# Kernel optimization log

Measured on AMD Instinct MI355X. Metric: run time of the kernel, lower is better.

## Reference

```python
import jax, jax.numpy as jnp
import numpy as np

N_NODES = 50000
N_EDGES = 800000
IN_FEATS = 128
NUM_HEADS = 4
OUT_FEATS = 16
NEG_SLOPE = 0.2


def setup_inputs() -> dict:
    key = jax.random.key(0)
    k1, k2, k3, k4, k5, k6, k7 = jax.random.split(key, 7)
    feat = jax.random.normal(k1, (N_NODES, IN_FEATS), dtype=jnp.float32)
    src = jax.random.randint(k2, (N_EDGES,), 0, N_NODES, dtype=jnp.int32)
    dst = jax.random.randint(k3, (N_EDGES,), 0, N_NODES, dtype=jnp.int32)
    edge_weight = jax.random.uniform(k4, (N_EDGES,), dtype=jnp.float32)
    W = jax.random.normal(k5, (IN_FEATS, NUM_HEADS * OUT_FEATS), dtype=jnp.float32) * 0.1
    attn_l = jax.random.normal(k6, (NUM_HEADS, OUT_FEATS), dtype=jnp.float32) * 0.1
    attn_r = jax.random.normal(k7, (NUM_HEADS, OUT_FEATS), dtype=jnp.float32) * 0.1
    return {"feat": feat, "src": src, "dst": dst, "edge_weight": edge_weight,
            "W": W, "attn_l": attn_l, "attn_r": attn_r}


def reference(feat, src, dst, edge_weight, W, attn_l, attn_r):
    N = feat.shape[0]
    # fc: [N, in] @ [in, H*D] -> [N, H, D]
    ft = (feat @ W).reshape(N, NUM_HEADS, OUT_FEATS)
    # per-node attention halves: [N, H]
    el = jnp.einsum('nhd,hd->nh', ft, attn_l)
    er = jnp.einsum('nhd,hd->nh', ft, attn_r)
    # edge scores: e_ij = edge_weight * leaky_relu(el[src] + er[dst])  -> [E, H]
    e = jax.nn.leaky_relu(el[src] + er[dst], negative_slope=NEG_SLOPE)
    e = edge_weight[:, None] * e
    # segmented softmax over incoming edges of each dst node
    emax = jax.ops.segment_max(e, dst, num_segments=N)           # [N, H]
    emax = jnp.where(jnp.isfinite(emax), emax, 0.0)              # guard isolated nodes
    expe = jnp.exp(e - emax[dst])                                # [E, H]
    denom = jax.ops.segment_sum(expe, dst, num_segments=N)       # [N, H]
    a = expe / denom[dst]                                        # [E, H]
    # weighted scatter-sum of source messages: [N, H, D]
    msg = ft[src] * a[:, :, None]
    rst = jax.ops.segment_sum(msg, dst, num_segments=N)
    return rst
```

## Files before the change

kernel.cpp:

```cpp
#include <hip/hip_runtime.h>
#include <hip/hip_bf16.h>

#define IN_F 128
#define NH   4
#define OD   16
#define HD   64
#define NEG  0.2f
#define LDP  136
#define SP   68
#define CAP  64
#define POISON ((int)0xAAAAAAAA)

#define BSH   7
#define NBUCK 391
#define CAPB  2560
#define EPB   4096

typedef float f32x4 __attribute__((ext_vector_type(4)));
typedef short bf16x8 __attribute__((ext_vector_type(8)));

__device__ __forceinline__ unsigned short f2bf(float f) {
  union { float f; unsigned u; } v; v.f = f;
  return (unsigned short)((v.u + 0x7fff + ((v.u >> 16) & 1)) >> 16);
}

__device__ __forceinline__ float bf2f(unsigned short b) {
  union { unsigned u; float f; } v; v.u = (unsigned)b << 16; return v.f;
}

__global__ __launch_bounds__(256) void fc_binscatter_kernel(
    const float* __restrict__ feat, const float* __restrict__ W,
    const float* __restrict__ attn_l, const float* __restrict__ attn_r,
    const int* __restrict__ src, const int* __restrict__ dst,
    const float* __restrict__ ew,
    __hip_bfloat16* __restrict__ ftb, float* __restrict__ el,
    float* __restrict__ er, int* __restrict__ bcnt,
    unsigned long long* __restrict__ ebuf,
    int N, int E, int GB) {
  const int t = threadIdx.x;
  __shared__ unsigned short Wtb[HD * LDP];
  __shared__ unsigned short Fb[64 * LDP];

  if (blockIdx.x >= GB) {
    int* hist  = (int*)Fb;
    int* gbase = hist + NBUCK;
    const int e0 = (blockIdx.x - GB) * EPB + t * 16;

    for (int b = t; b < NBUCK; b += 256) hist[b] = 0;
    __syncthreads();

    int dl[16];
    const bool full = (e0 + 16 <= E);
    if (full) {
      #pragma unroll
      for (int k = 0; k < 4; ++k) {
        const int4 d4 = *(const int4*)(dst + e0 + k * 4);
        dl[k*4+0] = d4.x; dl[k*4+1] = d4.y; dl[k*4+2] = d4.z; dl[k*4+3] = d4.w;
      }
      #pragma unroll
      for (int j = 0; j < 16; ++j) atomicAdd(&hist[dl[j] >> BSH], 1);
    } else if (e0 < E) {
      for (int j = 0; j < 16 && e0 + j < E; ++j) {
        dl[j] = dst[e0 + j];
        atomicAdd(&hist[dl[j] >> BSH], 1);
      }
    }
    __syncthreads();

    for (int b = t; b < NBUCK; b += 256) {
      const int c = hist[b];
      gbase[b] = c ? (atomicAdd(&bcnt[b], c) - POISON) : 0;
      hist[b] = 0;
    }
    __syncthreads();

    if (full) {
      int sa[16]; float wa[16];
      #pragma unroll
      for (int k = 0; k < 4; ++k) {
        const int4 s4 = *(const int4*)(src + e0 + k * 4);
        sa[k*4+0] = s4.x; sa[k*4+1] = s4.y; sa[k*4+2] = s4.z; sa[k*4+3] = s4.w;
        const float4 w4 = *(const float4*)(ew + e0 + k * 4);
        wa[k*4+0] = w4.x; wa[k*4+1] = w4.y; wa[k*4+2] = w4.z; wa[k*4+3] = w4.w;
      }
      #pragma unroll
      for (int j = 0; j < 16; ++j) {
        unsigned q = (unsigned)(wa[j] * 65536.f);
        if (q > 65535u) q = 65535u;
        const int b = dl[j] >> BSH;
        const int pos = gbase[b] + atomicAdd(&hist[b], 1);
        if (pos < CAPB)
          ebuf[(size_t)b * CAPB + pos] =
              ((unsigned long long)((unsigned)sa[j] | (q << 16)) << 32) |
              (unsigned)dl[j];
      }
    } else if (e0 < E) {
      for (int j = 0; j < 16 && e0 + j < E; ++j) {
        const int e = e0 + j;
        unsigned q = (unsigned)(ew[e] * 65536.f);
        if (q > 65535u) q = 65535u;
        const int b = dl[j] >> BSH;
        const int pos = gbase[b] + atomicAdd(&hist[b], 1);
        if (pos < CAPB)
          ebuf[(size_t)b * CAPB + pos] =
              ((unsigned long long)((unsigned)src[e] | (q << 16)) << 32) |
              (unsigned)dl[j];
      }
    }
    return;
  }

  const int group0 = blockIdx.x * 64;

  for (int i = t; i < IN_F * HD; i += 256) {
    const int k = i >> 6, c = i & 63;
    Fb[k * SP + c] = f2bf(W[i]);
  }
  __syncthreads();
  for (int i = t; i < IN_F * HD; i += 256) {
    const int k = i & 127, c = i >> 7;
    Wtb[c * LDP + k] = Fb[k * SP + c];
  }
  __syncthreads();
  for (int i = t; i < 64 * (IN_F / 8); i += 256) {
    const int nl = i >> 4, c8 = i & 15;
    const int n = group0 + nl;
    float4 u, v;
    if (n < N) {
      u = ((const float4*)(feat + (size_t)n * IN_F))[c8 * 2];
      v = ((const float4*)(feat + (size_t)n * IN_F))[c8 * 2 + 1];
    } else {
      u = v = make_float4(0.f, 0.f, 0.f, 0.f);
    }
    bf16x8 pk;
    pk[0] = (short)f2bf(u.x); pk[1] = (short)f2bf(u.y);
    pk[2] = (short)f2bf(u.z); pk[3] = (short)f2bf(u.w);
    pk[4] = (short)f2bf(v.x); pk[5] = (short)f2bf(v.y);
    pk[6] = (short)f2bf(v.z); pk[7] = (short)f2bf(v.w);
    *(bf16x8*)&Fb[nl * LDP + c8 * 8] = pk;
  }
  __syncthreads();

  const int wave = t >> 6;
  const int lane = t & 63;
  const int ln = lane & 15, q = lane >> 4;

  f32x4 acc[4] = {{0.f, 0.f, 0.f, 0.f}, {0.f, 0.f, 0.f, 0.f},
                  {0.f, 0.f, 0.f, 0.f}, {0.f, 0.f, 0.f, 0.f}};
  #pragma unroll
  for (int ks = 0; ks < 4; ++ks) {
    const bf16x8 a = *(const bf16x8*)&Fb[(wave * 16 + ln) * LDP + ks * 32 + q * 8];
    #pragma unroll
    for (int tt = 0; tt < 4; ++tt) {
      const bf16x8 b = *(const bf16x8*)&Wtb[(tt * 16 + ln) * LDP + ks * 32 + q * 8];
      acc[tt] = __builtin_amdgcn_mfma_f32_16x16x32_bf16(a, b, acc[tt], 0, 0, 0);
    }
  }

  float alv[4], arv[4];
  #pragma unroll
  for (int tt = 0; tt < 4; ++tt) {
    alv[tt] = attn_l[tt * OD + ln];
    arv[tt] = attn_r[tt * OD + ln];
  }
  #pragma unroll
  for (int r = 0; r < 4; ++r) {
    const int node = group0 + wave * 16 + q * 4 + r;
    const bool ok = node < N;
    #pragma unroll
    for (int tt = 0; tt < 4; ++tt) {
      const float val = acc[tt][r];
      if (ok) ftb[(size_t)node * HD + tt * 16 + ln] =
          __hip_bfloat16_raw{f2bf(val)};
      float xl = val * alv[tt], xr = val * arv[tt];
      #pragma unroll
      for (int off = 8; off > 0; off >>= 1) {
        xl += __shfl_down(xl, off, 16);
        xr += __shfl_down(xr, off, 16);
      }
      if (ok && ln == 0) {
        el[node * NH + tt] = xl;
        er[node * NH + tt] = xr;
      }
    }
  }
}

__global__ __launch_bounds__(256) void fill_kernel(
    const unsigned long long* __restrict__ ebuf,
    const int* __restrict__ bcnt, unsigned* __restrict__ sw,
    int* __restrict__ deg, int N) {
  __shared__ int h2[128];
  const int b = blockIdx.x, t = threadIdx.x;
  if (t < 128) h2[t] = 0;
  __syncthreads();
  int cnt = bcnt[b] - POISON;
  cnt = min(max(cnt, 0), CAPB);
  for (int i = t; i < cnt; i += 256) {
    const unsigned long long pk = ebuf[(size_t)b * CAPB + i];
    const int d = (int)(unsigned)pk;
    const unsigned srcw = (unsigned)(pk >> 32);
    const int pos = atomicAdd(&h2[d & 127], 1);
    if (pos < CAP) sw[(size_t)d * CAP + pos] = srcw;
  }
  __syncthreads();
  const int n = b * 128 + t;
  if (t < 128 && n < N) deg[n] = min(h2[t], CAP) + POISON;
}

__global__ __launch_bounds__(256) void aggregate_kernel(
    const int* __restrict__ deg, const unsigned* __restrict__ sw,
    const float* __restrict__ el, const float* __restrict__ er,
    const __hip_bfloat16* __restrict__ ftb, float* __restrict__ out, int N) {
  const int n = blockIdx.x * 4 + (threadIdx.x >> 6);
  if (n >= N) return;
  const int lane = threadIdx.x & 63;
  int dn = deg[n] - POISON;
  dn = min(max(dn, 0), CAP);
  const int jp = lane >> 2, hp = lane & 3;
  const int g = lane >> 4, sub = lane & 15;
  const int hsub = sub >> 2;
  const float er_own = er[n * NH + hp];
  const unsigned* swn = sw + (size_t)n * CAP;
  const unsigned short* ftw = (const unsigned short*)ftb;

  float a0 = 0.f, a1 = 0.f, a2 = 0.f, a3 = 0.f, den = 0.f;
  for (int i0 = 0; i0 < dn; i0 += 16) {
    const int m = dn - i0;
    unsigned pr = 0u;
    int sj = 0;
    float pv = 0.f;
    if (jp < m) {
      pr = swn[i0 + jp];
      sj = (int)(pr & 0xFFFFu);
      const float w = ((float)(pr >> 16) + 0.5f) * (1.f / 65536.f);
      float sc = el[sj * NH + hp] + er_own;
      sc = sc > 0.f ? sc : NEG * sc;
      pv = __expf(w * sc);
      den += pv;
    }
    #pragma unroll
    for (int c = 0; c < 4; ++c) {
      const int ec = c * 4 + g;
      const int   sg = __shfl(sj, ec * 4, 64);
      const float pg = __shfl(pv, ec * 4 + hsub, 64);
      float v0 = 0.f, v1 = 0.f, v2 = 0.f, v3 = 0.f;
      if (ec < m) {
        const ushort4 rv = *(const ushort4*)(ftw + (size_t)sg * HD + sub * 4);
        v0 = bf2f(rv.x); v1 = bf2f(rv.y); v2 = bf2f(rv.z); v3 = bf2f(rv.w);
      }
      a0 += pg * v0; a1 += pg * v1; a2 += pg * v2; a3 += pg * v3;
    }
  }
  den += __shfl_xor(den, 4, 64);
  den += __shfl_xor(den, 8, 64);
  den += __shfl_xor(den, 16, 64);
  den += __shfl_xor(den, 32, 64);
  const float denh = __shfl(den, hsub, 64);
  a0 += __shfl_xor(a0, 16, 64); a0 += __shfl_xor(a0, 32, 64);
  a1 += __shfl_xor(a1, 16, 64); a1 += __shfl_xor(a1, 32, 64);
  a2 += __shfl_xor(a2, 16, 64); a2 += __shfl_xor(a2, 32, 64);
  a3 += __shfl_xor(a3, 16, 64); a3 += __shfl_xor(a3, 32, 64);
  if (g == 0) {
    const float inv = (dn > 0 && denh > 0.f) ? 1.f / denh : 0.f;
    *(float4*)(out + (size_t)n * HD + sub * 4) =
        make_float4(a0 * inv, a1 * inv, a2 * inv, a3 * inv);
  }
}

extern "C" void kernel_launch(void* const* d_in, const int* in_sizes, int n_in,
                              void* d_out, int out_size, void* d_ws, size_t ws_size,
                              hipStream_t stream) {
  const float* feat   = (const float*)d_in[0];
  const int*   src    = (const int*)d_in[1];
  const int*   dst    = (const int*)d_in[2];
  const float* ew     = (const float*)d_in[3];
  const float* W      = (const float*)d_in[4];
  const float* attn_l = (const float*)d_in[5];
  const float* attn_r = (const float*)d_in[6];
  float* out = (float*)d_out;

  const int N  = in_sizes[0] / IN_F;
  const int E  = in_sizes[1];
  const int GB = (N + 63) / 64;
  const int SBB = (E + EPB - 1) / EPB;

  char* p = (char*)d_ws;
  __hip_bfloat16* ftb = (__hip_bfloat16*)p; p += (size_t)N * HD * 2;
  float*    el  = (float*)p;    p += (size_t)N * NH * 4;
  float*    er  = (float*)p;    p += (size_t)N * NH * 4;
  unsigned* sw  = (unsigned*)p; p += (size_t)N * CAP * 4;
  int*      deg = (int*)p;      p += (size_t)N * 4;
  unsigned long long* ebuf = (unsigned long long*)p;
  p += (size_t)NBUCK * CAPB * 8;
  int* bcnt = (int*)p;          p += (size_t)NBUCK * 4;

  fc_binscatter_kernel<<<GB + SBB, 256, 0, stream>>>(feat, W, attn_l, attn_r,
                                                     src, dst, ew,
                                                     ftb, el, er, bcnt, ebuf,
                                                     N, E, GB);
  fill_kernel<<<NBUCK, 256, 0, stream>>>(ebuf, bcnt, sw, deg, N);
  aggregate_kernel<<<(N + 3) / 4, 256, 0, stream>>>(deg, sw, el, er, ftb,
                                                    out, N);
}
```

Baseline: 136.6 us.

## Fuse bucket fill and aggregation into one kernel using LDS slot lists

Merges the fill kernel and the aggregate kernel into one kernel. Each 512-thread block scatters its bucket's edges into a 32KB shared-memory adjacency table and then aggregates its 128 destination nodes, 16 per wave. This removes the global sw/deg round trip and one kernel launch. In exchange there are only 391 blocks with heavy LDS use, so occupancy and parallelism drop sharply compared with the 12500-block aggregate launch, which may hurt latency hiding on the gathers.

```diff
diff --git a/kernel.cpp b/kernel.cpp
--- a/kernel.cpp
+++ b/kernel.cpp
@@ -12,6 +12,7 @@
 #define POISON ((int)0xAAAAAAAA)
 
 #define BSH   7
+#define BN    128
 #define NBUCK 391
 #define CAPB  2560
 #define EPB   4096
@@ -186,85 +187,85 @@
   }
 }
 
-__global__ __launch_bounds__(256) void fill_kernel(
+__global__ __launch_bounds__(512) void bucket_fill_aggregate_kernel(
     const unsigned long long* __restrict__ ebuf,
-    const int* __restrict__ bcnt, unsigned* __restrict__ sw,
-    int* __restrict__ deg, int N) {
-  __shared__ int h2[128];
+    const int* __restrict__ bcnt,
+    const float* __restrict__ el, const float* __restrict__ er,
+    const __hip_bfloat16* __restrict__ ftb, float* __restrict__ out, int N) {
+  __shared__ unsigned slots[BN * CAP];
+  __shared__ int h2[BN];
   const int b = blockIdx.x, t = threadIdx.x;
-  if (t < 128) h2[t] = 0;
-  __syncthreads();
+  const int node0 = b << BSH;
+
+  if (t < BN) h2[t] = 0;
+  __syncthreads();
+
   int cnt = bcnt[b] - POISON;
   cnt = min(max(cnt, 0), CAPB);
-  for (int i = t; i < cnt; i += 256) {
-    const unsigned long long pk = ebuf[(size_t)b * CAPB + i];
-    const int d = (int)(unsigned)pk;
+  const unsigned long long* eb = ebuf + (size_t)b * CAPB;
+  for (int i = t; i < cnt; i += 512) {
+    const unsigned long long pk = eb[i];
+    const int dl = (int)(unsigned)pk & (BN - 1);
     const unsigned srcw = (unsigned)(pk >> 32);
-    const int pos = atomicAdd(&h2[d & 127], 1);
-    if (pos < CAP) sw[(size_t)d * CAP + pos] = srcw;
-  }
-  __syncthreads();
-  const int n = b * 128 + t;
-  if (t < 128 && n < N) deg[n] = min(h2[t], CAP) + POISON;
-}
-
-__global__ __launch_bounds__(256) void aggregate_kernel(
-    const int* __restrict__ deg, const unsigned* __restrict__ sw,
-    const float* __restrict__ el, const float* __restrict__ er,
-    const __hip_bfloat16* __restrict__ ftb, float* __restrict__ out, int N) {
-  const int n = blockIdx.x * 4 + (threadIdx.x >> 6);
-  if (n >= N) return;
-  const int lane = threadIdx.x & 63;
-  int dn = deg[n] - POISON;
-  dn = min(max(dn, 0), CAP);
+    const int pos = atomicAdd(&h2[dl], 1);
+    if (pos < CAP) slots[dl * CAP + pos] = srcw;
+  }
+  __syncthreads();
+
+  const int wave = t >> 6, lane = t & 63;
   const int jp = lane >> 2, hp = lane & 3;
   const int g = lane >> 4, sub = lane & 15;
   const int hsub = sub >> 2;
-  const float er_own = er[n * NH + hp];
-  const unsigned* swn = sw + (size_t)n * CAP;
   const unsigned short* ftw = (const unsigned short*)ftb;
 
-  float a0 = 0.f, a1 = 0.f, a2 = 0.f, a3 = 0.f, den = 0.f;
-  for (int i0 = 0; i0 < dn; i0 += 16) {
-    const int m = dn - i0;
-    unsigned pr = 0u;
-    int sj = 0;
-    float pv = 0.f;
-    if (jp < m) {
-      pr = swn[i0 + jp];
-      sj = (int)(pr & 0xFFFFu);
-      const float w = ((float)(pr >> 16) + 0.5f) * (1.f / 65536.f);
-      float sc = el[sj * NH + hp] + er_own;
-      sc = sc > 0.f ? sc : NEG * sc;
-      pv = __expf(w * sc);
-      den += pv;
-    }
-    #pragma unroll
-    for (int c = 0; c < 4; ++c) {
-      const int ec = c * 4 + g;
-      const int   sg = __shfl(sj, ec * 4, 64);
-      const float pg = __shfl(pv, ec * 4 + hsub, 64);
-      float v0 = 0.f, v1 = 0.f, v2 = 0.f, v3 = 0.f;
-      if (ec < m) {
-        const ushort4 rv = *(const ushort4*)(ftw + (size_t)sg * HD + sub * 4);
-        v0 = bf2f(rv.x); v1 = bf2f(rv.y); v2 = bf2f(rv.z); v3 = bf2f(rv.w);
-      }
-      a0 += pg * v0; a1 += pg * v1; a2 += pg * v2; a3 += pg * v3;
-    }
-  }
-  den += __shfl_xor(den, 4, 64);
-  den += __shfl_xor(den, 8, 64);
-  den += __shfl_xor(den, 16, 64);
-  den += __shfl_xor(den, 32, 64);
-  const float denh = __shfl(den, hsub, 64);
-  a0 += __shfl_xor(a0, 16, 64); a0 += __shfl_xor(a0, 32, 64);
-  a1 += __shfl_xor(a1, 16, 64); a1 += __shfl_xor(a1, 32, 64);
-  a2 += __shfl_xor(a2, 16, 64); a2 += __shfl_xor(a2, 32, 64);
-  a3 += __shfl_xor(a3, 16, 64); a3 += __shfl_xor(a3, 32, 64);
-  if (g == 0) {
-    const float inv = (dn > 0 && denh > 0.f) ? 1.f / denh : 0.f;
-    *(float4*)(out + (size_t)n * HD + sub * 4) =
-        make_float4(a0 * inv, a1 * inv, a2 * inv, a3 * inv);
+  for (int v = 0; v < 16; ++v) {
+    const int ln = wave * 16 + v;
+    const int n = node0 + ln;
+    if (n >= N) break;
+    const int dn = min(h2[ln], CAP);
+    const float er_own = er[n * NH + hp];
+
+    float a0 = 0.f, a1 = 0.f, a2 = 0.f, a3 = 0.f, den = 0.f;
+    for (int i0 = 0; i0 < dn; i0 += 16) {
+      const int m = dn - i0;
+      int sj = 0;
+      float pv = 0.f;
+      if (jp < m) {
+        const unsigned pr = slots[ln * CAP + i0 + jp];
+        sj = (int)(pr & 0xFFFFu);
+        const float w = ((float)(pr >> 16) + 0.5f) * (1.f / 65536.f);
+        float sc = el[sj * NH + hp] + er_own;
+        sc = sc > 0.f ? sc : NEG * sc;
+        pv = __expf(w * sc);
+        den += pv;
+      }
+      #pragma unroll
+      for (int c = 0; c < 4; ++c) {
+        const int ec = c * 4 + g;
+        const int   sg = __shfl(sj, ec * 4, 64);
+        const float pg = __shfl(pv, ec * 4 + hsub, 64);
+        float v0 = 0.f, v1 = 0.f, v2 = 0.f, v3 = 0.f;
+        if (ec < m) {
+          const ushort4 rv = *(const ushort4*)(ftw + (size_t)sg * HD + sub * 4);
+          v0 = bf2f(rv.x); v1 = bf2f(rv.y); v2 = bf2f(rv.z); v3 = bf2f(rv.w);
+        }
+        a0 += pg * v0; a1 += pg * v1; a2 += pg * v2; a3 += pg * v3;
+      }
+    }
+    den += __shfl_xor(den, 4, 64);
+    den += __shfl_xor(den, 8, 64);
+    den += __shfl_xor(den, 16, 64);
+    den += __shfl_xor(den, 32, 64);
+    const float denh = __shfl(den, hsub, 64);
+    a0 += __shfl_xor(a0, 16, 64); a0 += __shfl_xor(a0, 32, 64);
+    a1 += __shfl_xor(a1, 16, 64); a1 += __shfl_xor(a1, 32, 64);
+    a2 += __shfl_xor(a2, 16, 64); a2 += __shfl_xor(a2, 32, 64);
+    a3 += __shfl_xor(a3, 16, 64); a3 += __shfl_xor(a3, 32, 64);
+    if (g == 0) {
+      const float inv = (dn > 0 && denh > 0.f) ? 1.f / denh : 0.f;
+      *(float4*)(out + (size_t)n * HD + sub * 4) =
+          make_float4(a0 * inv, a1 * inv, a2 * inv, a3 * inv);
+    }
   }
 }
 
@@ -289,8 +290,6 @@
   __hip_bfloat16* ftb = (__hip_bfloat16*)p; p += (size_t)N * HD * 2;
   float*    el  = (float*)p;    p += (size_t)N * NH * 4;
   float*    er  = (float*)p;    p += (size_t)N * NH * 4;
-  unsigned* sw  = (unsigned*)p; p += (size_t)N * CAP * 4;
-  int*      deg = (int*)p;      p += (size_t)N * 4;
   unsigned long long* ebuf = (unsigned long long*)p;
   p += (size_t)NBUCK * CAPB * 8;
   int* bcnt = (int*)p;          p += (size_t)NBUCK * 4;
@@ -299,7 +298,6 @@
                                                      src, dst, ew,
                                                      ftb, el, er, bcnt, ebuf,
                                                      N, E, GB);
-  fill_kernel<<<NBUCK, 256, 0, stream>>>(ebuf, bcnt, sw, deg, N);
-  aggregate_kernel<<<(N + 3) / 4, 256, 0, stream>>>(deg, sw, el, er, ftb,
-                                                    out, N);
-}
+  bucket_fill_aggregate_kernel<<<NBUCK, 512, 0, stream>>>(ebuf, bcnt, el, er,
+                                                          ftb, out, N);
+}
```

After: 151.5 us. +10.9%, slower.
